# Kernel optimization log

Hardware: AMD Instinct MI355X
Metric: run time of the kernel (lower is better)

Reference implementation:

```python
import jax, jax.numpy as jnp
import numpy as np

N_USER, N_ITEM = 100000, 50000
E, L = 640000, 200000
F0, F1, F2 = 128, 128, 64


def _mean_agg(x_src, src, dst, n_dst):
    # gather messages from source nodes, mean-aggregate onto destination nodes
    msg = x_src[src]                                            # [E, F]
    s = jax.ops.segment_sum(msg, dst, num_segments=n_dst)       # [n_dst, F]
    cnt = jax.ops.segment_sum(jnp.ones((src.shape[0], 1), x_src.dtype), dst,
                              num_segments=n_dst)               # [n_dst, 1]
    return s / jnp.maximum(cnt, 1.0)


def _sage(x_src, x_dst, src, dst, n_dst, Wl, b, Wr):
    # PyG SAGEConv: lin_l(mean_aggr(x_src)) + lin_r(x_dst)
    agg = _mean_agg(x_src, src, dst, n_dst)
    return agg @ Wl + b + x_dst @ Wr


def setup_inputs() -> dict:
    key = jax.random.key(0)
    ks = jax.random.split(key, 20)
    inp = {}
    inp['x_user'] = jax.random.normal(ks[0], (N_USER, F0), jnp.float32)
    inp['x_item'] = jax.random.normal(ks[1], (N_ITEM, F0), jnp.float32)
    inp['src_u'] = jax.random.randint(ks[2], (E,), 0, N_USER)
    inp['dst_i'] = jax.random.randint(ks[3], (E,), 0, N_ITEM)
    inp['el_src'] = jax.random.randint(ks[4], (L,), 0, N_USER)
    inp['el_dst'] = jax.random.randint(ks[5], (L,), 0, N_ITEM)
    # SAGEConv params per edge type per layer: Wl (neighbor), bias, Wr (root)
    def w(k, fi, fo):
        return jax.random.normal(k, (fi, fo), jnp.float32) * (1.0 / np.sqrt(fi))
    inp['Wl_ui1'] = w(ks[6], F0, F1);  inp['b_ui1'] = jnp.zeros((F1,), jnp.float32)
    inp['Wr_ui1'] = w(ks[7], F0, F1)
    inp['Wl_iu1'] = w(ks[8], F0, F1);  inp['b_iu1'] = jnp.zeros((F1,), jnp.float32)
    inp['Wr_iu1'] = w(ks[9], F0, F1)
    inp['Wl_ui2'] = w(ks[10], F1, F2); inp['b_ui2'] = jnp.zeros((F2,), jnp.float32)
    inp['Wr_ui2'] = w(ks[11], F1, F2)
    inp['Wl_iu2'] = w(ks[12], F1, F2); inp['b_iu2'] = jnp.zeros((F2,), jnp.float32)
    inp['Wr_iu2'] = w(ks[13], F1, F2)
    return inp


def reference(x_user, x_item, src_u, dst_i, el_src, el_dst,
              Wl_ui1, b_ui1, Wr_ui1, Wl_iu1, b_iu1, Wr_iu1,
              Wl_ui2, b_ui2, Wr_ui2, Wl_iu2, b_iu2, Wr_iu2):
    # layer 1 (to_hetero: one SAGEConv per edge type; relu per node type; eval -> no dropout)
    h_i1 = jax.nn.relu(_sage(x_user, x_item, src_u, dst_i, N_ITEM, Wl_ui1, b_ui1, Wr_ui1))
    h_u1 = jax.nn.relu(_sage(x_item, x_user, dst_i, src_u, N_USER, Wl_iu1, b_iu1, Wr_iu1))
    # layer 2
    h_i2 = _sage(h_u1, h_i1, src_u, dst_i, N_ITEM, Wl_ui2, b_ui2, Wr_ui2)
    h_u2 = _sage(h_i1, h_u1, dst_i, src_u, N_USER, Wl_iu2, b_iu2, Wr_iu2)
    # LPsimple_classif: gather endpoints, elementwise product, sum over features
    pred = (h_u2[el_src] * h_i2[el_dst]).sum(axis=-1)           # [L]
    return pred
```

## Files before the change

kernel.cpp:

```cpp
#include <hip/hip_runtime.h>

#define NUSER 100000
#define NITEM 50000
#define NEDGE 640000
#define NLINK 200000
#define GI 49
#define GU 98

typedef unsigned int  uint;
typedef unsigned short ushort_t;
typedef __attribute__((ext_vector_type(8))) short bf16x8;
typedef __attribute__((ext_vector_type(4))) float f32x4;
typedef __attribute__((ext_vector_type(4))) uint  u32x4;

__device__ __forceinline__ ushort_t f2bf(float f) {
    uint u = __float_as_uint(f);
    u += 0x7FFFu + ((u >> 16) & 1u);
    return (ushort_t)(u >> 16);
}
__device__ __forceinline__ float bf2f(ushort_t h) { return __uint_as_float(((uint)h) << 16); }
__device__ __forceinline__ float lo16f(uint u) { return __uint_as_float(u << 16); }
__device__ __forceinline__ float hi16f(uint u) { return __uint_as_float(u & 0xFFFF0000u); }

__global__ void count_kernel(const int* __restrict__ src, const int* __restrict__ dst,
                             int* __restrict__ cnt_u, int* __restrict__ cnt_i) {
    int e = blockIdx.x * blockDim.x + threadIdx.x;
    if (e >= NEDGE) return;
    atomicAdd(&cnt_u[src[e]], 1);
    atomicAdd(&cnt_i[dst[e]], 1);
}

__global__ __launch_bounds__(256) void scan1_kernel(
    const int* __restrict__ cnt_i, const int* __restrict__ cnt_u,
    int* __restrict__ head_i, int* __restrict__ head_u,
    int* __restrict__ bsum_i, int* __restrict__ bsum_u)
{
    __shared__ int sh[256];
    int b = blockIdx.x, t = threadIdx.x;
    const int* cnt; int* head; int* bsum; int n, cb;
    if (b < GI) { cnt = cnt_i; head = head_i; bsum = bsum_i; n = NITEM; cb = b; }
    else        { cnt = cnt_u; head = head_u; bsum = bsum_u; n = NUSER; cb = b - GI; }
    int base = cb * 1024 + t * 4;
    int4 v = {0, 0, 0, 0};
    if (base + 3 < n) v = *(const int4*)(cnt + base);
    else {
        if (base + 0 < n) v.x = cnt[base + 0];
        if (base + 1 < n) v.y = cnt[base + 1];
        if (base + 2 < n) v.z = cnt[base + 2];
    }
    int s = v.x + v.y + v.z + v.w;
    sh[t] = s;
    __syncthreads();
    for (int o = 1; o < 256; o <<= 1) {
        int a = (t >= o) ? sh[t - o] : 0;
        __syncthreads();
        sh[t] += a;
        __syncthreads();
    }
    int excl = sh[t] - s;
    if (t == 255) bsum[cb] = sh[255];
    if (base + 0 < n) head[base + 0] = excl;
    if (base + 1 < n) head[base + 1] = excl + v.x;
    if (base + 2 < n) head[base + 2] = excl + v.x + v.y;
    if (base + 3 < n) head[base + 3] = excl + v.x + v.y + v.z;
}

__global__ __launch_bounds__(256) void scan2_kernel(int* __restrict__ bsum_i,
                                                    int* __restrict__ bsum_u) {
    __shared__ int sh[256];
    int t = threadIdx.x;
    int orig = (t < GI) ? bsum_i[t] : 0;
    sh[t] = orig; __syncthreads();
    for (int o = 1; o < 256; o <<= 1) {
        int a = (t >= o) ? sh[t - o] : 0; __syncthreads(); sh[t] += a; __syncthreads();
    }
    if (t < GI) bsum_i[t] = sh[t] - orig;
    __syncthreads();
    int orig2 = (t < GU) ? bsum_u[t] : 0;
    sh[t] = orig2; __syncthreads();
    for (int o = 1; o < 256; o <<= 1) {
        int a = (t >= o) ? sh[t - o] : 0; __syncthreads(); sh[t] += a; __syncthreads();
    }
    if (t < GU) bsum_u[t] = sh[t] - orig2;
}

__global__ __launch_bounds__(256) void scan3_kernel(
    int* __restrict__ head_i, int* __restrict__ head_u,
    const int* __restrict__ bsum_i, const int* __restrict__ bsum_u)
{
    int b = blockIdx.x, t = threadIdx.x;
    int* head; const int* bsum; int n, cb;
    if (b < GI) { head = head_i; bsum = bsum_i; n = NITEM; cb = b; }
    else        { head = head_u; bsum = bsum_u; n = NUSER; cb = b - GI; }
    int add = bsum[cb];
    int base = cb * 1024 + t * 4;
#pragma unroll
    for (int k = 0; k < 4; ++k)
        if (base + k < n) head[base + k] += add;
}

#define FCHUNK 2048
#define FNCH   313
__global__ __launch_bounds__(256) void fillb_kernel(
    const int* __restrict__ src, const int* __restrict__ dst,
    int* __restrict__ head_i, int* __restrict__ head_u,
    int* __restrict__ nbr_i, int* __restrict__ nbr_u)
{
    int b = blockIdx.x;
    int pass = b / (2 * FNCH);
    int rem  = b % (2 * FNCH);
    int dir  = rem / FNCH;
    int base = (rem % FNCH) * FCHUNK;
    int e_end = min(base + FCHUNK, NEDGE);
    if (dir == 0) {
        int lo = pass * (NITEM / 8), hi = lo + NITEM / 8;
        for (int e = base + threadIdx.x; e < e_end; e += 256) {
            int d = dst[e];
            if (d >= lo && d < hi) nbr_i[atomicAdd(&head_i[d], 1)] = src[e];
        }
    } else {
        int lo = pass * (NUSER / 8), hi = lo + NUSER / 8;
        for (int e = base + threadIdx.x; e < e_end; e += 256) {
            int s = src[e];
            if (s >= lo && s < hi) nbr_u[atomicAdd(&head_u[s], 1)] = dst[e];
        }
    }
}

__global__ __launch_bounds__(256) void wprep_kernel(
    const float* __restrict__ Wl0, const float* __restrict__ Wr0,
    const float* __restrict__ Wl1, const float* __restrict__ Wr1,
    const float* __restrict__ Wl2, const float* __restrict__ Wr2,
    const float* __restrict__ Wl3, const float* __restrict__ Wr3,
    ushort_t* __restrict__ Bh0, ushort_t* __restrict__ Bl0,
    ushort_t* __restrict__ Bh1, ushort_t* __restrict__ Bl1,
    ushort_t* __restrict__ Bh2, ushort_t* __restrict__ Bl2,
    ushort_t* __restrict__ Bh3, ushort_t* __restrict__ Bl3)
{
    int b = blockIdx.x;
    const float *Wl, *Wr; ushort_t *Bh, *Bl; int FO, t;
    if (b < 16)      { Wl = Wl0; Wr = Wr0; Bh = Bh0; Bl = Bl0; FO = 128; t = b * 256 + threadIdx.x; }
    else if (b < 32) { Wl = Wl1; Wr = Wr1; Bh = Bh1; Bl = Bl1; FO = 128; t = (b - 16) * 256 + threadIdx.x; }
    else if (b < 40) { Wl = Wl2; Wr = Wr2; Bh = Bh2; Bl = Bl2; FO = 64;  t = (b - 32) * 256 + threadIdx.x; }
    else             { Wl = Wl3; Wr = Wr3; Bh = Bh3; Bl = Bl3; FO = 64;  t = (b - 40) * 256 + threadIdx.x; }
    int lane = t & 63, ks = (t >> 6) & 3, nt = t >> 8;
    int col = nt * 16 + (lane & 15);
    int k0 = ks * 32 + (lane >> 4) * 8;
    const float* W = (col < FO) ? Wl : Wr;
    int cc = (col < FO) ? col : col - FO;
#pragma unroll
    for (int j = 0; j < 8; ++j) {
        float v = W[(size_t)(k0 + j) * FO + cc];
        ushort_t h = f2bf(v);
        Bh[(size_t)t * 8 + j] = h;
        Bl[(size_t)t * 8 + j] = f2bf(v - bf2f(h));
    }
}

template <int NO, bool ASPLIT>
__global__ __launch_bounds__(256) void gemm_kernel(
    const void* __restrict__ A0, const void* __restrict__ A1,
    const ushort_t* __restrict__ Bh0, const ushort_t* __restrict__ Bl0,
    const ushort_t* __restrict__ Bh1, const ushort_t* __restrict__ Bl1,
    ushort_t* __restrict__ y0, ushort_t* __restrict__ z0,
    ushort_t* __restrict__ y1, ushort_t* __restrict__ z1,
    int n0, int n1, int nb0)
{
    constexpr int CT = NO / 64;
    constexpr int FO = NO / 2;
    __shared__ u32x4 ashH[32][16];
    __shared__ u32x4 ashL[ASPLIT ? 32 : 1][16];
    const int tid = threadIdx.x;
    const void* A_; const ushort_t *Bh, *Bl; ushort_t *ymsg, *zout; int n, row0;
    if ((int)blockIdx.x < nb0) { A_ = A0; Bh = Bh0; Bl = Bl0; ymsg = y0; zout = z0; n = n0; row0 = blockIdx.x * 32; }
    else { A_ = A1; Bh = Bh1; Bl = Bl1; ymsg = y1; zout = z1; n = n1; row0 = (blockIdx.x - nb0) * 32; }

    if (ASPLIT) {
        const float* A = (const float*)A_;
#pragma unroll
        for (int i = 0; i < 2; ++i) {
            int idx = i * 256 + tid;
            int row = idx >> 4, ch = idx & 15;
            int grow = row0 + row;
            f32x4 f0 = {0.f, 0.f, 0.f, 0.f}, f1 = {0.f, 0.f, 0.f, 0.f};
            if (grow < n) {
                const f32x4* p = (const f32x4*)((const float*)A + (size_t)grow * 128 + ch * 8);
                f0 = p[0]; f1 = p[1];
            }
            float e[8];
#pragma unroll
            for (int j = 0; j < 4; ++j) { e[j] = f0[j]; e[4 + j] = f1[j]; }
            uint hv[4], lv[4];
#pragma unroll
            for (int j = 0; j < 4; ++j) {
                ushort_t h0 = f2bf(e[2 * j]), h1 = f2bf(e[2 * j + 1]);
                hv[j] = (uint)h0 | ((uint)h1 << 16);
                ushort_t l0 = f2bf(e[2 * j] - bf2f(h0)), l1 = f2bf(e[2 * j + 1] - bf2f(h1));
                lv[j] = (uint)l0 | ((uint)l1 << 16);
            }
            int sc = ch ^ (row & 7);
            u32x4 hq = {hv[0], hv[1], hv[2], hv[3]};
            u32x4 lq = {lv[0], lv[1], lv[2], lv[3]};
            ashH[row][sc] = hq;
            ashL[row][sc] = lq;
        }
    } else {
        const ushort_t* A = (const ushort_t*)A_;
#pragma unroll
        for (int i = 0; i < 2; ++i) {
            int idx = i * 256 + tid;
            int row = idx >> 4, ch = idx & 15;
            int grow = row0 + row;
            u32x4 q = {0u, 0u, 0u, 0u};
            if (grow < n) q = *(const u32x4*)(A + (size_t)grow * 128 + ch * 8);
            ashH[row][ch ^ (row & 7)] = q;
        }
    }
    __syncthreads();

    const int lane = tid & 63, wv = tid >> 6;
    const int lr = lane & 15, lg = lane >> 4;
    const int colbase = wv * (NO / 4);
    f32x4 acc[2][CT];
#pragma unroll
    for (int rt = 0; rt < 2; ++rt)
#pragma unroll
        for (int ct = 0; ct < CT; ++ct) { f32x4 zz = {0.f, 0.f, 0.f, 0.f}; acc[rt][ct] = zz; }

#pragma unroll
    for (int ks = 0; ks < 4; ++ks) {
        bf16x8 ah[2], al[2];
#pragma unroll
        for (int rt = 0; rt < 2; ++rt) {
            int row = rt * 16 + lr;
            int pos = (ks * 4 + lg) ^ (row & 7);
            ah[rt] = __builtin_bit_cast(bf16x8, ashH[row][pos]);
            if (ASPLIT) al[rt] = __builtin_bit_cast(bf16x8, ashL[row][pos]);
        }
#pragma unroll
        for (int ct = 0; ct < CT; ++ct) {
            int nt = (colbase >> 4) + ct;
            size_t off = ((size_t)(nt * 4 + ks) * 64 + lane) * 8;
            bf16x8 bh = __builtin_bit_cast(bf16x8, *(const u32x4*)(Bh + off));
            bf16x8 bl = __builtin_bit_cast(bf16x8, *(const u32x4*)(Bl + off));
#pragma unroll
            for (int rt = 0; rt < 2; ++rt) {
                acc[rt][ct] = __builtin_amdgcn_mfma_f32_16x16x32_bf16(ah[rt], bh, acc[rt][ct], 0, 0, 0);
                acc[rt][ct] = __builtin_amdgcn_mfma_f32_16x16x32_bf16(ah[rt], bl, acc[rt][ct], 0, 0, 0);
                if (ASPLIT)
                    acc[rt][ct] = __builtin_amdgcn_mfma_f32_16x16x32_bf16(al[rt], bh, acc[rt][ct], 0, 0, 0);
            }
        }
    }

#pragma unroll
    for (int rt = 0; rt < 2; ++rt)
#pragma unroll
        for (int ct = 0; ct < CT; ++ct) {
            int col = colbase + ct * 16 + lr;
            bool ism = col < FO;
            ushort_t* dst = ism ? ymsg : zout;
            int cc = ism ? col : col - FO;
#pragma unroll
            for (int r = 0; r < 4; ++r) {
                int row = row0 + rt * 16 + lg * 4 + r;
                if (row < n) dst[(size_t)row * FO + cc] = f2bf(acc[rt][ct][r]);
            }
        }
}

__global__ __launch_bounds__(256) void gather1_kernel(
    const ushort_t* __restrict__ ymsg_u, const ushort_t* __restrict__ ymsg_i,
    const int* __restrict__ nbr_i, const int* __restrict__ head_i, const int* __restrict__ cnt_i,
    const int* __restrict__ nbr_u, const int* __restrict__ head_u, const int* __restrict__ cnt_u,
    const ushort_t* __restrict__ z_i, const ushort_t* __restrict__ z_u,
    const float* __restrict__ b_ui, const float* __restrict__ b_iu,
    ushort_t* __restrict__ h1_i, ushort_t* __restrict__ h1_u)
{
    int w = (blockIdx.x << 2) + (threadIdx.x >> 6);
    const ushort_t *ym, *z; const int *nbr, *head, *cnt; const float* bias;
    ushort_t* hout; int node;
    if (w < NITEM) { ym = ymsg_u; nbr = nbr_i; head = head_i; cnt = cnt_i; z = z_i; bias = b_ui; hout = h1_i; node = w; }
    else if (w < NITEM + NUSER) { ym = ymsg_i; nbr = nbr_u; head = head_u; cnt = cnt_u; z = z_u; bias = b_iu; hout = h1_u; node = w - NITEM; }
    else return;
    int lane = threadIdx.x & 63;
    int c = cnt[node], end = head[node];
    int j = end - c;
    const uint* Y = (const uint*)ym;
    float ax = 0.f, ay = 0.f;
    for (; j + 7 < end; j += 8) {
        uint u0 = Y[(size_t)nbr[j + 0] * 64 + lane];
        uint u1 = Y[(size_t)nbr[j + 1] * 64 + lane];
        uint u2 = Y[(size_t)nbr[j + 2] * 64 + lane];
        uint u3 = Y[(size_t)nbr[j + 3] * 64 + lane];
        uint u4 = Y[(size_t)nbr[j + 4] * 64 + lane];
        uint u5 = Y[(size_t)nbr[j + 5] * 64 + lane];
        uint u6 = Y[(size_t)nbr[j + 6] * 64 + lane];
        uint u7 = Y[(size_t)nbr[j + 7] * 64 + lane];
        ax += lo16f(u0) + lo16f(u1) + lo16f(u2) + lo16f(u3)
            + lo16f(u4) + lo16f(u5) + lo16f(u6) + lo16f(u7);
        ay += hi16f(u0) + hi16f(u1) + hi16f(u2) + hi16f(u3)
            + hi16f(u4) + hi16f(u5) + hi16f(u6) + hi16f(u7);
    }
    for (; j + 1 < end; j += 2) {
        uint u0 = Y[(size_t)nbr[j + 0] * 64 + lane];
        uint u1 = Y[(size_t)nbr[j + 1] * 64 + lane];
        ax += lo16f(u0) + lo16f(u1);
        ay += hi16f(u0) + hi16f(u1);
    }
    if (j < end) {
        uint u0 = Y[(size_t)nbr[j] * 64 + lane];
        ax += lo16f(u0); ay += hi16f(u0);
    }
    float m = 1.f / fmaxf((float)c, 1.f);
    uint zu = ((const uint*)z)[(size_t)node * 64 + lane];
    float vx = fmaxf(ax * m + lo16f(zu) + bias[lane * 2], 0.f);
    float vy = fmaxf(ay * m + hi16f(zu) + bias[lane * 2 + 1], 0.f);
    ((uint*)hout)[(size_t)node * 64 + lane] = (uint)f2bf(vx) | ((uint)f2bf(vy) << 16);
}

__global__ __launch_bounds__(256) void gather2_kernel(
    const ushort_t* __restrict__ ymsg_u, const ushort_t* __restrict__ ymsg_i,
    const int* __restrict__ nbr_i, const int* __restrict__ head_i, const int* __restrict__ cnt_i,
    const int* __restrict__ nbr_u, const int* __restrict__ head_u, const int* __restrict__ cnt_u,
    const ushort_t* __restrict__ z_i, const ushort_t* __restrict__ z_u,
    const float* __restrict__ b_ui, const float* __restrict__ b_iu,
    ushort_t* __restrict__ h2_i, ushort_t* __restrict__ h2_u)
{
    int w = (blockIdx.x << 2) + (threadIdx.x >> 6);
    const ushort_t *ym, *z; const int *nbr, *head, *cnt; const float* bias;
    ushort_t* hout; int node;
    if (w < NITEM) { ym = ymsg_u; nbr = nbr_i; head = head_i; cnt = cnt_i; z = z_i; bias = b_ui; hout = h2_i; node = w; }
    else if (w < NITEM + NUSER) { ym = ymsg_i; nbr = nbr_u; head = head_u; cnt = cnt_u; z = z_u; bias = b_iu; hout = h2_u; node = w - NITEM; }
    else return;
    int lane = threadIdx.x & 63;
    int c = cnt[node], end = head[node];
    int j = end - c;
    float a = 0.f;
    for (; j + 7 < end; j += 8) {
        a += bf2f(ym[(size_t)nbr[j + 0] * 64 + lane]) + bf2f(ym[(size_t)nbr[j + 1] * 64 + lane])
           + bf2f(ym[(size_t)nbr[j + 2] * 64 + lane]) + bf2f(ym[(size_t)nbr[j + 3] * 64 + lane])
           + bf2f(ym[(size_t)nbr[j + 4] * 64 + lane]) + bf2f(ym[(size_t)nbr[j + 5] * 64 + lane])
           + bf2f(ym[(size_t)nbr[j + 6] * 64 + lane]) + bf2f(ym[(size_t)nbr[j + 7] * 64 + lane]);
    }
    for (; j + 1 < end; j += 2)
        a += bf2f(ym[(size_t)nbr[j] * 64 + lane]) + bf2f(ym[(size_t)nbr[j + 1] * 64 + lane]);
    if (j < end) a += bf2f(ym[(size_t)nbr[j] * 64 + lane]);
    float m = 1.f / fmaxf((float)c, 1.f);
    float v = a * m + bf2f(z[(size_t)node * 64 + lane]) + bias[lane];
    hout[(size_t)node * 64 + lane] = f2bf(v);
}

__global__ __launch_bounds__(256) void predict_kernel(
    const int* __restrict__ el_src, const int* __restrict__ el_dst,
    const ushort_t* __restrict__ hu, const ushort_t* __restrict__ hi,
    float* __restrict__ out)
{
    int l = (blockIdx.x << 2) + (threadIdx.x >> 6);
    if (l >= NLINK) return;
    int lane = threadIdx.x & 63;
    int u = el_src[l];
    int it = el_dst[l];
    float v = bf2f(hu[(size_t)u * 64 + lane]) * bf2f(hi[(size_t)it * 64 + lane]);
#pragma unroll
    for (int o = 32; o >= 1; o >>= 1) v += __shfl_down(v, o, 64);
    if (lane == 0) out[l] = v;
}

extern "C" void kernel_launch(void* const* d_in, const int* in_sizes, int n_in,
                              void* d_out, int out_size, void* d_ws, size_t ws_size,
                              hipStream_t stream) {
    const float* x_user = (const float*)d_in[0];
    const float* x_item = (const float*)d_in[1];
    const int*   src_u  = (const int*)d_in[2];
    const int*   dst_i  = (const int*)d_in[3];
    const int*   el_src = (const int*)d_in[4];
    const int*   el_dst = (const int*)d_in[5];
    const float* Wl_ui1 = (const float*)d_in[6];
    const float* b_ui1  = (const float*)d_in[7];
    const float* Wr_ui1 = (const float*)d_in[8];
    const float* Wl_iu1 = (const float*)d_in[9];
    const float* b_iu1  = (const float*)d_in[10];
    const float* Wr_iu1 = (const float*)d_in[11];
    const float* Wl_ui2 = (const float*)d_in[12];
    const float* b_ui2  = (const float*)d_in[13];
    const float* Wr_ui2 = (const float*)d_in[14];
    const float* Wl_iu2 = (const float*)d_in[15];
    const float* b_iu2  = (const float*)d_in[16];
    const float* Wr_iu2 = (const float*)d_in[17];
    float* out = (float*)d_out;

    int* iw     = (int*)d_ws;
    int* cnt_i  = iw;
    int* cnt_u  = iw + 50000;
    int* bsum_i = iw + 150000;
    int* bsum_u = iw + 150064;
    int* head_i = iw + 150192;
    int* head_u = iw + 200192;
    int* nbr_i  = iw + 300192;
    int* nbr_u  = iw + 940192;
    char* W8 = (char*)d_ws;
    size_t off = 6320768;
    ushort_t* Bh1u = (ushort_t*)(W8 + off); off += 65536;
    ushort_t* Bl1u = (ushort_t*)(W8 + off); off += 65536;
    ushort_t* Bh1i = (ushort_t*)(W8 + off); off += 65536;
    ushort_t* Bl1i = (ushort_t*)(W8 + off); off += 65536;
    ushort_t* Bh2u = (ushort_t*)(W8 + off); off += 32768;
    ushort_t* Bl2u = (ushort_t*)(W8 + off); off += 32768;
    ushort_t* Bh2i = (ushort_t*)(W8 + off); off += 32768;
    ushort_t* Bl2i = (ushort_t*)(W8 + off); off += 32768;
    ushort_t* h1_u = (ushort_t*)(W8 + off); off += (size_t)NUSER * 128 * 2;
    ushort_t* h1_i = (ushort_t*)(W8 + off); off += (size_t)NITEM * 128 * 2;
    size_t YB = off;
    ushort_t* ymsg_u = (ushort_t*)(W8 + YB);
    ushort_t* ymsg_i = (ushort_t*)(W8 + YB + 25600000);
    ushort_t* z_u    = (ushort_t*)(W8 + YB + 38400000);
    ushort_t* z_i    = (ushort_t*)(W8 + YB + 64000000);
    ushort_t* ymsg2_u = (ushort_t*)(W8 + YB);
    ushort_t* ymsg2_i = (ushort_t*)(W8 + YB + 12800000);
    ushort_t* z2_u    = (ushort_t*)(W8 + YB + 19200000);
    ushort_t* z2_i    = (ushort_t*)(W8 + YB + 32000000);
    ushort_t* h2_u    = (ushort_t*)(W8 + YB + 38400000);
    ushort_t* h2_i    = (ushort_t*)(W8 + YB + 51200000);
    size_t total_ws = YB + 76800000;

    hipMemsetAsync(d_ws, 0, total_ws, stream);

    count_kernel<<<(NEDGE + 255) / 256, 256, 0, stream>>>(src_u, dst_i, cnt_u, cnt_i);
    scan1_kernel<<<GI + GU, 256, 0, stream>>>(cnt_i, cnt_u, head_i, head_u, bsum_i, bsum_u);
    scan2_kernel<<<1, 256, 0, stream>>>(bsum_i, bsum_u);
    scan3_kernel<<<GI + GU, 256, 0, stream>>>(head_i, head_u, bsum_i, bsum_u);
    fillb_kernel<<<8 * 2 * FNCH, 256, 0, stream>>>(src_u, dst_i, head_i, head_u, nbr_i, nbr_u);

    wprep_kernel<<<48, 256, 0, stream>>>(Wl_ui1, Wr_iu1, Wl_iu1, Wr_ui1,
                                         Wl_ui2, Wr_iu2, Wl_iu2, Wr_ui2,
                                         Bh1u, Bl1u, Bh1i, Bl1i,
                                         Bh2u, Bl2u, Bh2i, Bl2i);

    gemm_kernel<256, true><<<3125 + 1563, 256, 0, stream>>>(
        x_user, x_item, Bh1u, Bl1u, Bh1i, Bl1i,
        ymsg_u, z_u, ymsg_i, z_i, NUSER, NITEM, 3125);
    gather1_kernel<<<(NITEM + NUSER) / 4, 256, 0, stream>>>(
        ymsg_u, ymsg_i, nbr_i, head_i, cnt_i, nbr_u, head_u, cnt_u,
        z_i, z_u, b_ui1, b_iu1, h1_i, h1_u);

    gemm_kernel<128, false><<<3125 + 1563, 256, 0, stream>>>(
        h1_u, h1_i, Bh2u, Bl2u, Bh2i, Bl2i,
        ymsg2_u, z2_u, ymsg2_i, z2_i, NUSER, NITEM, 3125);
    gather2_kernel<<<(NITEM + NUSER) / 4, 256, 0, stream>>>(
        ymsg2_u, ymsg2_i, nbr_i, head_i, cnt_i, nbr_u, head_u, cnt_u,
        z2_i, z2_u, b_ui2, b_iu2, h2_i, h2_u);

    predict_kernel<<<NLINK / 4, 256, 0, stream>>>(el_src, el_dst, h2_u, h2_i, out);
}
```

Measured before the change: 379.3 us.

## Fuse graph-build kernels with weight prep and layer-1 GEMM, shrink workspace memset

```diff
diff --git a/kernel.cpp b/kernel.cpp
--- a/kernel.cpp
+++ b/kernel.cpp
@@ -22,12 +22,43 @@
 __device__ __forceinline__ float lo16f(uint u) { return __uint_as_float(u << 16); }
 __device__ __forceinline__ float hi16f(uint u) { return __uint_as_float(u & 0xFFFF0000u); }
 
-__global__ void count_kernel(const int* __restrict__ src, const int* __restrict__ dst,
-                             int* __restrict__ cnt_u, int* __restrict__ cnt_i) {
-    int e = blockIdx.x * blockDim.x + threadIdx.x;
-    if (e >= NEDGE) return;
-    atomicAdd(&cnt_u[src[e]], 1);
-    atomicAdd(&cnt_i[dst[e]], 1);
+__global__ __launch_bounds__(256) void countw_kernel(
+    const int* __restrict__ src, const int* __restrict__ dst,
+    int* __restrict__ cnt_u, int* __restrict__ cnt_i,
+    const float* __restrict__ Wl0, const float* __restrict__ Wr0,
+    const float* __restrict__ Wl1, const float* __restrict__ Wr1,
+    const float* __restrict__ Wl2, const float* __restrict__ Wr2,
+    const float* __restrict__ Wl3, const float* __restrict__ Wr3,
+    ushort_t* __restrict__ Bh0, ushort_t* __restrict__ Bl0,
+    ushort_t* __restrict__ Bh1, ushort_t* __restrict__ Bl1,
+    ushort_t* __restrict__ Bh2, ushort_t* __restrict__ Bl2,
+    ushort_t* __restrict__ Bh3, ushort_t* __restrict__ Bl3)
+{
+    if (blockIdx.x < 2500) {
+        int e = blockIdx.x * 256 + threadIdx.x;
+        if (e >= NEDGE) return;
+        atomicAdd(&cnt_u[src[e]], 1);
+        atomicAdd(&cnt_i[dst[e]], 1);
+        return;
+    }
+    int b = blockIdx.x - 2500;
+    const float *Wl, *Wr; ushort_t *Bh, *Bl; int FO, t;
+    if (b < 16)      { Wl = Wl0; Wr = Wr0; Bh = Bh0; Bl = Bl0; FO = 128; t = b * 256 + threadIdx.x; }
+    else if (b < 32) { Wl = Wl1; Wr = Wr1; Bh = Bh1; Bl = Bl1; FO = 128; t = (b - 16) * 256 + threadIdx.x; }
+    else if (b < 40) { Wl = Wl2; Wr = Wr2; Bh = Bh2; Bl = Bl2; FO = 64;  t = (b - 32) * 256 + threadIdx.x; }
+    else             { Wl = Wl3; Wr = Wr3; Bh = Bh3; Bl = Bl3; FO = 64;  t = (b - 40) * 256 + threadIdx.x; }
+    int lane = t & 63, ks = (t >> 6) & 3, nt = t >> 8;
+    int col = nt * 16 + (lane & 15);
+    int k0 = ks * 32 + (lane >> 4) * 8;
+    const float* W = (col < FO) ? Wl : Wr;
+    int cc = (col < FO) ? col : col - FO;
+#pragma unroll
+    for (int j = 0; j < 8; ++j) {
+        float v = W[(size_t)(k0 + j) * FO + cc];
+        ushort_t h = f2bf(v);
+        Bh[(size_t)t * 8 + j] = h;
+        Bl[(size_t)t * 8 + j] = f2bf(v - bf2f(h));
+    }
 }
 
 __global__ __launch_bounds__(256) void scan1_kernel(
@@ -65,34 +96,22 @@
     if (base + 3 < n) head[base + 3] = excl + v.x + v.y + v.z;
 }
 
-__global__ __launch_bounds__(256) void scan2_kernel(int* __restrict__ bsum_i,
-                                                    int* __restrict__ bsum_u) {
-    __shared__ int sh[256];
-    int t = threadIdx.x;
-    int orig = (t < GI) ? bsum_i[t] : 0;
-    sh[t] = orig; __syncthreads();
-    for (int o = 1; o < 256; o <<= 1) {
-        int a = (t >= o) ? sh[t - o] : 0; __syncthreads(); sh[t] += a; __syncthreads();
-    }
-    if (t < GI) bsum_i[t] = sh[t] - orig;
-    __syncthreads();
-    int orig2 = (t < GU) ? bsum_u[t] : 0;
-    sh[t] = orig2; __syncthreads();
-    for (int o = 1; o < 256; o <<= 1) {
-        int a = (t >= o) ? sh[t - o] : 0; __syncthreads(); sh[t] += a; __syncthreads();
-    }
-    if (t < GU) bsum_u[t] = sh[t] - orig2;
-}
-
-__global__ __launch_bounds__(256) void scan3_kernel(
+__global__ __launch_bounds__(256) void scan23_kernel(
     int* __restrict__ head_i, int* __restrict__ head_u,
     const int* __restrict__ bsum_i, const int* __restrict__ bsum_u)
 {
+    __shared__ int sh[256];
     int b = blockIdx.x, t = threadIdx.x;
     int* head; const int* bsum; int n, cb;
     if (b < GI) { head = head_i; bsum = bsum_i; n = NITEM; cb = b; }
     else        { head = head_u; bsum = bsum_u; n = NUSER; cb = b - GI; }
-    int add = bsum[cb];
+    sh[t] = (t < cb) ? bsum[t] : 0;
+    __syncthreads();
+    for (int o = 128; o >= 1; o >>= 1) {
+        if (t < o) sh[t] += sh[t + o];
+        __syncthreads();
+    }
+    int add = sh[0];
     int base = cb * 1024 + t * 4;
 #pragma unroll
     for (int k = 0; k < 4; ++k)
@@ -101,144 +120,171 @@
 
 #define FCHUNK 2048
 #define FNCH   313
-__global__ __launch_bounds__(256) void fillb_kernel(
+#define NBG1   4688
+__global__ __launch_bounds__(256) void gemmfill_kernel(
+    const float* __restrict__ xu, const float* __restrict__ xi,
+    const ushort_t* __restrict__ Bh0, const ushort_t* __restrict__ Bl0,
+    const ushort_t* __restrict__ Bh1, const ushort_t* __restrict__ Bl1,
+    ushort_t* __restrict__ y0, ushort_t* __restrict__ z0,
+    ushort_t* __restrict__ y1, ushort_t* __restrict__ z1,
     const int* __restrict__ src, const int* __restrict__ dst,
     int* __restrict__ head_i, int* __restrict__ head_u,
     int* __restrict__ nbr_i, int* __restrict__ nbr_u)
 {
-    int b = blockIdx.x;
-    int pass = b / (2 * FNCH);
-    int rem  = b % (2 * FNCH);
-    int dir  = rem / FNCH;
-    int base = (rem % FNCH) * FCHUNK;
-    int e_end = min(base + FCHUNK, NEDGE);
-    if (dir == 0) {
-        int lo = pass * (NITEM / 8), hi = lo + NITEM / 8;
-        for (int e = base + threadIdx.x; e < e_end; e += 256) {
-            int d = dst[e];
-            if (d >= lo && d < hi) nbr_i[atomicAdd(&head_i[d], 1)] = src[e];
-        }
-    } else {
-        int lo = pass * (NUSER / 8), hi = lo + NUSER / 8;
-        for (int e = base + threadIdx.x; e < e_end; e += 256) {
-            int s = src[e];
-            if (s >= lo && s < hi) nbr_u[atomicAdd(&head_u[s], 1)] = dst[e];
-        }
-    }
-}
-
-__global__ __launch_bounds__(256) void wprep_kernel(
-    const float* __restrict__ Wl0, const float* __restrict__ Wr0,
-    const float* __restrict__ Wl1, const float* __restrict__ Wr1,
-    const float* __restrict__ Wl2, const float* __restrict__ Wr2,
-    const float* __restrict__ Wl3, const float* __restrict__ Wr3,
-    ushort_t* __restrict__ Bh0, ushort_t* __restrict__ Bl0,
-    ushort_t* __restrict__ Bh1, ushort_t* __restrict__ Bl1,
-    ushort_t* __restrict__ Bh2, ushort_t* __restrict__ Bl2,
-    ushort_t* __restrict__ Bh3, ushort_t* __restrict__ Bl3)
-{
-    int b = blockIdx.x;
-    const float *Wl, *Wr; ushort_t *Bh, *Bl; int FO, t;
-    if (b < 16)      { Wl = Wl0; Wr = Wr0; Bh = Bh0; Bl = Bl0; FO = 128; t = b * 256 + threadIdx.x; }
-    else if (b < 32) { Wl = Wl1; Wr = Wr1; Bh = Bh1; Bl = Bl1; FO = 128; t = (b - 16) * 256 + threadIdx.x; }
-    else if (b < 40) { Wl = Wl2; Wr = Wr2; Bh = Bh2; Bl = Bl2; FO = 64;  t = (b - 32) * 256 + threadIdx.x; }
-    else             { Wl = Wl3; Wr = Wr3; Bh = Bh3; Bl = Bl3; FO = 64;  t = (b - 40) * 256 + threadIdx.x; }
-    int lane = t & 63, ks = (t >> 6) & 3, nt = t >> 8;
-    int col = nt * 16 + (lane & 15);
-    int k0 = ks * 32 + (lane >> 4) * 8;
-    const float* W = (col < FO) ? Wl : Wr;
-    int cc = (col < FO) ? col : col - FO;
-#pragma unroll
-    for (int j = 0; j < 8; ++j) {
-        float v = W[(size_t)(k0 + j) * FO + cc];
-        ushort_t h = f2bf(v);
-        Bh[(size_t)t * 8 + j] = h;
-        Bl[(size_t)t * 8 + j] = f2bf(v - bf2f(h));
-    }
-}
-
-template <int NO, bool ASPLIT>
-__global__ __launch_bounds__(256) void gemm_kernel(
-    const void* __restrict__ A0, const void* __restrict__ A1,
+    if (blockIdx.x >= NBG1) {
+        int b = blockIdx.x - NBG1;
+        int pass = b / (2 * FNCH);
+        int rem  = b % (2 * FNCH);
+        int dir  = rem / FNCH;
+        int base = (rem % FNCH) * FCHUNK;
+        int e_end = min(base + FCHUNK, NEDGE);
+        if (dir == 0) {
+            int lo = pass * (NITEM / 8), hi = lo + NITEM / 8;
+            for (int e = base + threadIdx.x; e < e_end; e += 256) {
+                int d = dst[e];
+                if (d >= lo && d < hi) nbr_i[atomicAdd(&head_i[d], 1)] = src[e];
+            }
+        } else {
+            int lo = pass * (NUSER / 8), hi = lo + NUSER / 8;
+            for (int e = base + threadIdx.x; e < e_end; e += 256) {
+                int s = src[e];
+                if (s >= lo && s < hi) nbr_u[atomicAdd(&head_u[s], 1)] = dst[e];
+            }
+        }
+        return;
+    }
+
+    __shared__ u32x4 ashH[32][16];
+    __shared__ u32x4 ashL[32][16];
+    const int tid = threadIdx.x;
+    const float* A; const ushort_t *Bh, *Bl; ushort_t *ymsg, *zout; int n, row0;
+    if ((int)blockIdx.x < 3125) { A = xu; Bh = Bh0; Bl = Bl0; ymsg = y0; zout = z0; n = NUSER; row0 = blockIdx.x * 32; }
+    else { A = xi; Bh = Bh1; Bl = Bl1; ymsg = y1; zout = z1; n = NITEM; row0 = (blockIdx.x - 3125) * 32; }
+
+#pragma unroll
+    for (int i = 0; i < 2; ++i) {
+        int idx = i * 256 + tid;
+        int row = idx >> 4, ch = idx & 15;
+        int grow = row0 + row;
+        f32x4 f0 = {0.f, 0.f, 0.f, 0.f}, f1 = {0.f, 0.f, 0.f, 0.f};
+        if (grow < n) {
+            const f32x4* p = (const f32x4*)(A + (size_t)grow * 128 + ch * 8);
+            f0 = p[0]; f1 = p[1];
+        }
+        float e[8];
+#pragma unroll
+        for (int j = 0; j < 4; ++j) { e[j] = f0[j]; e[4 + j] = f1[j]; }
+        uint hv[4], lv[4];
+#pragma unroll
+        for (int j = 0; j < 4; ++j) {
+            ushort_t h0 = f2bf(e[2 * j]), h1 = f2bf(e[2 * j + 1]);
+            hv[j] = (uint)h0 | ((uint)h1 << 16);
+            ushort_t l0 = f2bf(e[2 * j] - bf2f(h0)), l1 = f2bf(e[2 * j + 1] - bf2f(h1));
+            lv[j] = (uint)l0 | ((uint)l1 << 16);
+        }
+        int sc = ch ^ (row & 7);
+        u32x4 hq = {hv[0], hv[1], hv[2], hv[3]};
+        u32x4 lq = {lv[0], lv[1], lv[2], lv[3]};
+        ashH[row][sc] = hq;
+        ashL[row][sc] = lq;
+    }
+    __syncthreads();
+
+    const int lane = tid & 63, wv = tid >> 6;
+    const int lr = lane & 15, lg = lane >> 4;
+    const int colbase = wv * 64;
+    f32x4 acc[2][4];
+#pragma unroll
+    for (int rt = 0; rt < 2; ++rt)
+#pragma unroll
+        for (int ct = 0; ct < 4; ++ct) { f32x4 zz = {0.f, 0.f, 0.f, 0.f}; acc[rt][ct] = zz; }
+
+#pragma unroll
+    for (int ks = 0; ks < 4; ++ks) {
+        bf16x8 ah[2], al[2];
+#pragma unroll
+        for (int rt = 0; rt < 2; ++rt) {
+            int row = rt * 16 + lr;
+            int pos = (ks * 4 + lg) ^ (row & 7);
+            ah[rt] = __builtin_bit_cast(bf16x8, ashH[row][pos]);
+            al[rt] = __builtin_bit_cast(bf16x8, ashL[row][pos]);
+        }
+#pragma unroll
+        for (int ct = 0; ct < 4; ++ct) {
+            int nt = (colbase >> 4) + ct;
+            size_t off = ((size_t)(nt * 4 + ks) * 64 + lane) * 8;
+            bf16x8 bh = __builtin_bit_cast(bf16x8, *(const u32x4*)(Bh + off));
+            bf16x8 bl = __builtin_bit_cast(bf16x8, *(const u32x4*)(Bl + off));
+#pragma unroll
+            for (int rt = 0; rt < 2; ++rt) {
+                acc[rt][ct] = __builtin_amdgcn_mfma_f32_16x16x32_bf16(ah[rt], bh, acc[rt][ct], 0, 0, 0);
+                acc[rt][ct] = __builtin_amdgcn_mfma_f32_16x16x32_bf16(ah[rt], bl, acc[rt][ct], 0, 0, 0);
+                acc[rt][ct] = __builtin_amdgcn_mfma_f32_16x16x32_bf16(al[rt], bh, acc[rt][ct], 0, 0, 0);
+            }
+        }
+    }
+
+#pragma unroll
+    for (int rt = 0; rt < 2; ++rt)
+#pragma unroll
+        for (int ct = 0; ct < 4; ++ct) {
+            int col = colbase + ct * 16 + lr;
+            bool ism = col < 128;
+            ushort_t* dstp = ism ? ymsg : zout;
+            int cc = ism ? col : col - 128;
+#pragma unroll
+            for (int r = 0; r < 4; ++r) {
+                int row = row0 + rt * 16 + lg * 4 + r;
+                if (row < n) dstp[(size_t)row * 128 + cc] = f2bf(acc[rt][ct][r]);
+            }
+        }
+}
+
+__global__ __launch_bounds__(256) void gemm2_kernel(
+    const ushort_t* __restrict__ A0, const ushort_t* __restrict__ A1,
     const ushort_t* __restrict__ Bh0, const ushort_t* __restrict__ Bl0,
     const ushort_t* __restrict__ Bh1, const ushort_t* __restrict__ Bl1,
     ushort_t* __restrict__ y0, ushort_t* __restrict__ z0,
     ushort_t* __restrict__ y1, ushort_t* __restrict__ z1,
     int n0, int n1, int nb0)
 {
-    constexpr int CT = NO / 64;
-    constexpr int FO = NO / 2;
     __shared__ u32x4 ashH[32][16];
-    __shared__ u32x4 ashL[ASPLIT ? 32 : 1][16];
     const int tid = threadIdx.x;
-    const void* A_; const ushort_t *Bh, *Bl; ushort_t *ymsg, *zout; int n, row0;
-    if ((int)blockIdx.x < nb0) { A_ = A0; Bh = Bh0; Bl = Bl0; ymsg = y0; zout = z0; n = n0; row0 = blockIdx.x * 32; }
-    else { A_ = A1; Bh = Bh1; Bl = Bl1; ymsg = y1; zout = z1; n = n1; row0 = (blockIdx.x - nb0) * 32; }
-
-    if (ASPLIT) {
-        const float* A = (const float*)A_;
-#pragma unroll
-        for (int i = 0; i < 2; ++i) {
-            int idx = i * 256 + tid;
-            int row = idx >> 4, ch = idx & 15;
-            int grow = row0 + row;
-            f32x4 f0 = {0.f, 0.f, 0.f, 0.f}, f1 = {0.f, 0.f, 0.f, 0.f};
-            if (grow < n) {
-                const f32x4* p = (const f32x4*)((const float*)A + (size_t)grow * 128 + ch * 8);
-                f0 = p[0]; f1 = p[1];
-            }
-            float e[8];
-#pragma unroll
-            for (int j = 0; j < 4; ++j) { e[j] = f0[j]; e[4 + j] = f1[j]; }
-            uint hv[4], lv[4];
-#pragma unroll
-            for (int j = 0; j < 4; ++j) {
-                ushort_t h0 = f2bf(e[2 * j]), h1 = f2bf(e[2 * j + 1]);
-                hv[j] = (uint)h0 | ((uint)h1 << 16);
-                ushort_t l0 = f2bf(e[2 * j] - bf2f(h0)), l1 = f2bf(e[2 * j + 1] - bf2f(h1));
-                lv[j] = (uint)l0 | ((uint)l1 << 16);
-            }
-            int sc = ch ^ (row & 7);
-            u32x4 hq = {hv[0], hv[1], hv[2], hv[3]};
-            u32x4 lq = {lv[0], lv[1], lv[2], lv[3]};
-            ashH[row][sc] = hq;
-            ashL[row][sc] = lq;
-        }
-    } else {
-        const ushort_t* A = (const ushort_t*)A_;
-#pragma unroll
-        for (int i = 0; i < 2; ++i) {
-            int idx = i * 256 + tid;
-            int row = idx >> 4, ch = idx & 15;
-            int grow = row0 + row;
-            u32x4 q = {0u, 0u, 0u, 0u};
-            if (grow < n) q = *(const u32x4*)(A + (size_t)grow * 128 + ch * 8);
-            ashH[row][ch ^ (row & 7)] = q;
-        }
+    const ushort_t* A; const ushort_t *Bh, *Bl; ushort_t *ymsg, *zout; int n, row0;
+    if ((int)blockIdx.x < nb0) { A = A0; Bh = Bh0; Bl = Bl0; ymsg = y0; zout = z0; n = n0; row0 = blockIdx.x * 32; }
+    else { A = A1; Bh = Bh1; Bl = Bl1; ymsg = y1; zout = z1; n = n1; row0 = (blockIdx.x - nb0) * 32; }
+
+#pragma unroll
+    for (int i = 0; i < 2; ++i) {
+        int idx = i * 256 + tid;
+        int row = idx >> 4, ch = idx & 15;
+        int grow = row0 + row;
+        u32x4 q = {0u, 0u, 0u, 0u};
+        if (grow < n) q = *(const u32x4*)(A + (size_t)grow * 128 + ch * 8);
+        ashH[row][ch ^ (row & 7)] = q;
     }
     __syncthreads();
 
     const int lane = tid & 63, wv = tid >> 6;
     const int lr = lane & 15, lg = lane >> 4;
-    const int colbase = wv * (NO / 4);
-    f32x4 acc[2][CT];
+    const int colbase = wv * 32;
+    f32x4 acc[2][2];
 #pragma unroll
     for (int rt = 0; rt < 2; ++rt)
 #pragma unroll
-        for (int ct = 0; ct < CT; ++ct) { f32x4 zz = {0.f, 0.f, 0.f, 0.f}; acc[rt][ct] = zz; }
+        for (int ct = 0; ct < 2; ++ct) { f32x4 zz = {0.f, 0.f, 0.f, 0.f}; acc[rt][ct] = zz; }
 
 #pragma unroll
     for (int ks = 0; ks < 4; ++ks) {
-        bf16x8 ah[2], al[2];
+        bf16x8 ah[2];
 #pragma unroll
         for (int rt = 0; rt < 2; ++rt) {
             int row = rt * 16 + lr;
             int pos = (ks * 4 + lg) ^ (row & 7);
             ah[rt] = __builtin_bit_cast(bf16x8, ashH[row][pos]);
-            if (ASPLIT) al[rt] = __builtin_bit_cast(bf16x8, ashL[row][pos]);
-        }
-#pragma unroll
-        for (int ct = 0; ct < CT; ++ct) {
+        }
+#pragma unroll
+        for (int ct = 0; ct < 2; ++ct) {
             int nt = (colbase >> 4) + ct;
             size_t off = ((size_t)(nt * 4 + ks) * 64 + lane) * 8;
             bf16x8 bh = __builtin_bit_cast(bf16x8, *(const u32x4*)(Bh + off));
@@ -247,8 +293,6 @@
             for (int rt = 0; rt < 2; ++rt) {
                 acc[rt][ct] = __builtin_amdgcn_mfma_f32_16x16x32_bf16(ah[rt], bh, acc[rt][ct], 0, 0, 0);
                 acc[rt][ct] = __builtin_amdgcn_mfma_f32_16x16x32_bf16(ah[rt], bl, acc[rt][ct], 0, 0, 0);
-                if (ASPLIT)
-                    acc[rt][ct] = __builtin_amdgcn_mfma_f32_16x16x32_bf16(al[rt], bh, acc[rt][ct], 0, 0, 0);
             }
         }
     }
@@ -256,15 +300,15 @@
 #pragma unroll
     for (int rt = 0; rt < 2; ++rt)
 #pragma unroll
-        for (int ct = 0; ct < CT; ++ct) {
+        for (int ct = 0; ct < 2; ++ct) {
             int col = colbase + ct * 16 + lr;
-            bool ism = col < FO;
-            ushort_t* dst = ism ? ymsg : zout;
-            int cc = ism ? col : col - FO;
+            bool ism = col < 64;
+            ushort_t* dstp = ism ? ymsg : zout;
+            int cc = ism ? col : col - 64;
 #pragma unroll
             for (int r = 0; r < 4; ++r) {
                 int row = row0 + rt * 16 + lg * 4 + r;
-                if (row < n) dst[(size_t)row * FO + cc] = f2bf(acc[rt][ct][r]);
+                if (row < n) dstp[(size_t)row * 64 + cc] = f2bf(acc[rt][ct][r]);
             }
         }
 }
@@ -422,29 +466,27 @@
     ushort_t* z2_i    = (ushort_t*)(W8 + YB + 32000000);
     ushort_t* h2_u    = (ushort_t*)(W8 + YB + 38400000);
     ushort_t* h2_i    = (ushort_t*)(W8 + YB + 51200000);
-    size_t total_ws = YB + 76800000;
-
-    hipMemsetAsync(d_ws, 0, total_ws, stream);
-
-    count_kernel<<<(NEDGE + 255) / 256, 256, 0, stream>>>(src_u, dst_i, cnt_u, cnt_i);
+
+    hipMemsetAsync(d_ws, 0, 150000 * sizeof(int), stream);
+
+    countw_kernel<<<2548, 256, 0, stream>>>(
+        src_u, dst_i, cnt_u, cnt_i,
+        Wl_ui1, Wr_iu1, Wl_iu1, Wr_ui1, Wl_ui2, Wr_iu2, Wl_iu2, Wr_ui2,
+        Bh1u, Bl1u, Bh1i, Bl1i, Bh2u, Bl2u, Bh2i, Bl2i);
+
     scan1_kernel<<<GI + GU, 256, 0, stream>>>(cnt_i, cnt_u, head_i, head_u, bsum_i, bsum_u);
-    scan2_kernel<<<1, 256, 0, stream>>>(bsum_i, bsum_u);
-    scan3_kernel<<<GI + GU, 256, 0, stream>>>(head_i, head_u, bsum_i, bsum_u);
-    fillb_kernel<<<8 * 2 * FNCH, 256, 0, stream>>>(src_u, dst_i, head_i, head_u, nbr_i, nbr_u);
-
-    wprep_kernel<<<48, 256, 0, stream>>>(Wl_ui1, Wr_iu1, Wl_iu1, Wr_ui1,
-                                         Wl_ui2, Wr_iu2, Wl_iu2, Wr_ui2,
-                                         Bh1u, Bl1u, Bh1i, Bl1i,
-                                         Bh2u, Bl2u, Bh2i, Bl2i);
-
-    gemm_kernel<256, true><<<3125 + 1563, 256, 0, stream>>>(
+    scan23_kernel<<<GI + GU, 256, 0, stream>>>(head_i, head_u, bsum_i, bsum_u);
+
+    gemmfill_kernel<<<NBG1 + 8 * 2 * FNCH, 256, 0, stream>>>(
         x_user, x_item, Bh1u, Bl1u, Bh1i, Bl1i,
-        ymsg_u, z_u, ymsg_i, z_i, NUSER, NITEM, 3125);
+        ymsg_u, z_u, ymsg_i, z_i,
+        src_u, dst_i, head_i, head_u, nbr_i, nbr_u);
+
     gather1_kernel<<<(NITEM + NUSER) / 4, 256, 0, stream>>>(
         ymsg_u, ymsg_i, nbr_i, head_i, cnt_i, nbr_u, head_u, cnt_u,
         z_i, z_u, b_ui1, b_iu1, h1_i, h1_u);
 
-    gemm_kernel<128, false><<<3125 + 1563, 256, 0, stream>>>(
+    gemm2_kernel<<<3125 + 1563, 256, 0, stream>>>(
         h1_u, h1_i, Bh2u, Bl2u, Bh2i, Bl2i,
         ymsg2_u, z2_u, ymsg2_i, z2_i, NUSER, NITEM, 3125);
     gather2_kernel<<<(NITEM + NUSER) / 4, 256, 0, stream>>>(
```

Result: faster. 353.5 us (-6.8%).
